# Kernel tuning notes

Hardware: AMD Instinct MI355X
Metric: run time of the kernel (lower is better)

## Reference

```python
import jax, jax.numpy as jnp
import numpy as np
from jax import lax

H = 128          # lstm hidden size
IN = 128         # time_steps == LSTM input_size
NUM_LAYERS = 3   # num_variables
B = 512          # batch
S = 512          # sequence length


def _lstm_layer(x_tbi, Wih, Whh, bih, bhh):
    """x_tbi: (T, B, in). PyTorch gate order i, f, g, o. Returns (T, B, H), (hT, cT)."""
    T, Bb, _ = x_tbi.shape
    Hh = Whh.shape[1]
    # precompute input contribution to gates outside the scan
    xg = jnp.einsum('tbi,gi->tbg', x_tbi, Wih) + bih + bhh  # (T, B, 4H)

    def step(carry, xg_t):
        h, c = carry
        g = xg_t + h @ Whh.T                                # (B, 4H)
        i, f, gg, o = jnp.split(g, 4, axis=-1)
        c = jax.nn.sigmoid(f) * c + jax.nn.sigmoid(i) * jnp.tanh(gg)
        h = jax.nn.sigmoid(o) * jnp.tanh(c)
        return (h, c), h

    h0 = jnp.zeros((Bb, Hh), x_tbi.dtype)
    c0 = jnp.zeros((Bb, Hh), x_tbi.dtype)
    (hT, cT), ys = lax.scan(step, (h0, c0), xg)
    return ys, (hT, cT)


def setup_inputs() -> dict:
    key = jax.random.key(0)
    ks = jax.random.split(key, 1 + 4 * NUM_LAYERS)
    inp = {"x": jax.random.normal(ks[0], (B, S, IN), dtype=jnp.float32)}
    k = 1.0 / np.sqrt(H)
    ki = 1
    for l in range(NUM_LAYERS):
        in_dim = IN if l == 0 else H
        inp[f"Wih{l}"] = jax.random.uniform(ks[ki], (4 * H, in_dim), jnp.float32, -k, k); ki += 1
        inp[f"Whh{l}"] = jax.random.uniform(ks[ki], (4 * H, H), jnp.float32, -k, k); ki += 1
        inp[f"bih{l}"] = jax.random.uniform(ks[ki], (4 * H,), jnp.float32, -k, k); ki += 1
        inp[f"bhh{l}"] = jax.random.uniform(ks[ki], (4 * H,), jnp.float32, -k, k); ki += 1
    return inp


def reference(x, Wih0, Whh0, bih0, bhh0, Wih1, Whh1, bih1, bhh1, Wih2, Whh2, bih2, bhh2):
    # x: (B, S, IN) -> (S, B, IN), stacked LSTM, output (S, B, H)
    h = jnp.transpose(x, (1, 0, 2))
    params = [(Wih0, Whh0, bih0, bhh0), (Wih1, Whh1, bih1, bhh1), (Wih2, Whh2, bih2, bhh2)]
    for (Wih, Whh, bih, bhh) in params:
        h, _ = _lstm_layer(h, Wih, Whh, bih, bhh)
    # y = output.transpose(1, 2): (S, B, H) -> (S, H, B); dropout is identity in eval
    return jnp.transpose(h, (0, 2, 1))
```

## Files before the change

kernel.cpp:

```cpp
#include <hip/hip_runtime.h>
#include <stdint.h>

#define BATCH 512
#define SEQ   512
#define HID   128
#define BT    16
#define ROWB  528
#define NTILE 32
#define CH    8
#define RING  64
#define FPAD  32
#define SKEW  8

typedef _Float16 half8 __attribute__((ext_vector_type(8)));
typedef float f32x4 __attribute__((ext_vector_type(4)));
typedef unsigned long long u64;

union UHP { uint32_t u; _Float16 h[2]; };
__device__ __forceinline__ uint32_t pack2f(float a, float b){
  UHP r; r.h[0] = (_Float16)a; r.h[1] = (_Float16)b; return r.u;
}
__device__ __forceinline__ float unpk(uint32_t u, int i){
  UHP r; r.u = u; return (float)r.h[i];
}

__device__ __forceinline__ float rcp_(float x){
#if __has_builtin(__builtin_amdgcn_rcpf)
  return __builtin_amdgcn_rcpf(x);
#else
  return 1.f / x;
#endif
}
__device__ __forceinline__ float exp2_(float x){
#if __has_builtin(__builtin_amdgcn_exp2f)
  return __builtin_amdgcn_exp2f(x);
#else
  return exp2f(x);
#endif
}
__device__ __forceinline__ float sigm(float x){ return rcp_(1.f + exp2_(x * -1.44269504f)); }
__device__ __forceinline__ float tanh_(float x){ return 1.f - 2.f * rcp_(exp2_(x * 2.88539008f) + 1.f); }

__device__ __forceinline__ int aload(const int* p){
  return __hip_atomic_load(p, __ATOMIC_RELAXED, __HIP_MEMORY_SCOPE_AGENT);
}

template<int MODE>
__device__ __forceinline__ void run_layer(
    const float* __restrict__ Wih, const float* __restrict__ Whh,
    const float* __restrict__ bih, const float* __restrict__ bhh,
    const float* __restrict__ x, uint32_t* __restrict__ rin,
    uint32_t* __restrict__ rout, float* __restrict__ y,
    int* src_ready, int* src_done, int* dst_ready, int* dst_done,
    int b0, char* act0, char* act1)
{
  const int tid  = threadIdx.x;
  const int lane = tid & 63;
  const int w    = tid >> 6;
  const int u0   = w * 16;
  const int rm   = lane & 15;
  const int kq   = lane >> 4;

  half8 wf[4][8];
  #pragma unroll
  for (int g = 0; g < 4; ++g){
    const int grow = g * HID + u0 + rm;
    #pragma unroll
    for (int s = 0; s < 8; ++s){
      const int k = s * 32 + kq * 8;
      const float* src = (s < 4) ? (Wih + (size_t)grow * HID + k)
                                 : (Whh + (size_t)grow * HID + (k - HID));
      const float4 aa = *(const float4*)src;
      const float4 bb = *(const float4*)(src + 4);
      half8 hh;
      hh[0]=(_Float16)aa.x; hh[1]=(_Float16)aa.y; hh[2]=(_Float16)aa.z; hh[3]=(_Float16)aa.w;
      hh[4]=(_Float16)bb.x; hh[5]=(_Float16)bb.y; hh[6]=(_Float16)bb.z; hh[7]=(_Float16)bb.w;
      wf[g][s] = hh;
    }
  }
  f32x4 bias4[4];
  #pragma unroll
  for (int g = 0; g < 4; ++g)
    #pragma unroll
    for (int r = 0; r < 4; ++r){
      const int row = g * HID + u0 + kq * 4 + r;
      bias4[g][r] = bih[row] + bhh[row];
    }

  const int sb = tid >> 5;
  const int sk = tid & 31;

  auto xaddr = [&](int t){
    return (const float4*)(x + ((size_t)(b0 + sb) * SEQ + t) * HID + sk * 4);
  };
  auto raddr = [&](int t){
    return (u64*)(rin + ((size_t)(t & (RING-1)) * BATCH + b0 + sb) * 64 + sk * 2);
  };

  float4 pfa, pfb;
  u64    pga = 0, pgb = 0;

  int fseen = 0, fpend = 0, dseen = 0;

  if constexpr (MODE != 0){
    fseen = aload(src_ready);
    while (fseen < SKEW){ __builtin_amdgcn_s_sleep(8); fseen = aload(src_ready); }
  }
  if constexpr (MODE == 0){
    const float4 v = *xaddr(0);
    uint2 p; p.x = pack2f(v.x, v.y); p.y = pack2f(v.z, v.w);
    *(uint2*)(act0 + sb * ROWB + sk * 8) = p;
    pfa = *xaddr(1);
  } else {
    const u64 v = __hip_atomic_load(raddr(0), __ATOMIC_RELAXED, __HIP_MEMORY_SCOPE_AGENT);
    *(u64*)(act0 + sb * ROWB + sk * 8) = v;
    pga = __hip_atomic_load(raddr(1), __ATOMIC_RELAXED, __HIP_MEMORY_SCOPE_AGENT);
    fpend = aload(src_ready);
  }
  if (tid < 256)
    *(uint4*)(act0 + (tid >> 4) * ROWB + 256 + (tid & 15) * 16) = make_uint4(0u,0u,0u,0u);
  __syncthreads();

  f32x4 c4 = {0.f, 0.f, 0.f, 0.f};
  const int boff = rm * ROWB + kq * 16;
  int cur = 0;

  uint2 hp = {0u, 0u};

  for (int t = 0; t < SEQ; ++t){
    char* bc = cur ? act1 : act0;
    char* bn = cur ? act0 : act1;
    const int tn   = t + 1;
    const int tpre = t + 2;

    if (t > 0){
      if constexpr (MODE != 2){
        const u64 hp64 = ((u64)hp.y << 32) | (u64)hp.x;
        u64* p = (u64*)(rout + ((size_t)((t-1) & (RING-1)) * BATCH + b0 + rm) * 64 + (u0 >> 1) + kq * 2);
        __hip_atomic_store(p, hp64, __ATOMIC_RELAXED, __HIP_MEMORY_SCOPE_AGENT);
      } else {
        const size_t yb = ((size_t)(t-1) * HID + u0 + kq * 4) * BATCH + b0 + rm;
        y[yb]             = unpk(hp.x, 0);
        y[yb + BATCH]     = unpk(hp.x, 1);
        y[yb + 2 * BATCH] = unpk(hp.y, 0);
        y[yb + 3 * BATCH] = unpk(hp.y, 1);
      }
    }
    if (tid == 0){
      if constexpr (MODE != 2){
        if (t >= 2)
          __hip_atomic_store(dst_ready, t - 1, __ATOMIC_RELAXED, __HIP_MEMORY_SCOPE_AGENT);
      }
      if constexpr (MODE != 0){
        if ((t & (CH-1)) == 0 && t > 0)
          __hip_atomic_store(src_done, t >> 3, __ATOMIC_RELAXED, __HIP_MEMORY_SCOPE_AGENT);
      }
    }
    if constexpr (MODE != 2){
      if ((t & (CH-1)) == 0 && t >= RING){
        const int need = (t >> 3) - 7;
        if (dseen < need){
          dseen = aload(dst_done);
          while (dseen < need){ __builtin_amdgcn_s_sleep(8); dseen = aload(dst_done); }
        }
      }
    }
    if constexpr (MODE != 0){
      const int fnew = fpend;
      if (fnew > fseen) fseen = fnew;
      fpend = aload(src_ready);
      if (tpre < SEQ && fseen < tpre + 1){
        fseen = aload(src_ready);
        while (fseen < tpre + 1){ __builtin_amdgcn_s_sleep(2); fseen = aload(src_ready); }
      }
    }
    if (tpre < SEQ){
      if constexpr (MODE == 0) pfb = *xaddr(tpre);
      else pgb = __hip_atomic_load(raddr(tpre), __ATOMIC_RELAXED, __HIP_MEMORY_SCOPE_AGENT);
    }

    f32x4 a0 = bias4[0], a1 = bias4[1], a2 = bias4[2], a3 = bias4[3];
    #pragma unroll
    for (int s = 0; s < 8; ++s){
      const half8 bf = *(const half8*)(bc + boff + s * 64);
      a0 = __builtin_amdgcn_mfma_f32_16x16x32_f16(wf[0][s], bf, a0, 0, 0, 0);
      a1 = __builtin_amdgcn_mfma_f32_16x16x32_f16(wf[1][s], bf, a1, 0, 0, 0);
      a2 = __builtin_amdgcn_mfma_f32_16x16x32_f16(wf[2][s], bf, a2, 0, 0, 0);
      a3 = __builtin_amdgcn_mfma_f32_16x16x32_f16(wf[3][s], bf, a3, 0, 0, 0);
    }

    float hvr[4];
    #pragma unroll
    for (int r = 0; r < 4; ++r){
      const float ii = sigm(a0[r]), ff = sigm(a1[r]);
      const float gg = tanh_(a2[r]), oo = sigm(a3[r]);
      c4[r] = ff * c4[r] + ii * gg;
      hvr[r] = oo * tanh_(c4[r]);
    }
    hp.x = pack2f(hvr[0], hvr[1]);
    hp.y = pack2f(hvr[2], hvr[3]);

    *(uint2*)(bn + rm * ROWB + 256 + u0 * 2 + kq * 8) = hp;
    if (tn < SEQ){
      if constexpr (MODE == 0){
        uint2 p; p.x = pack2f(pfa.x, pfa.y); p.y = pack2f(pfa.z, pfa.w);
        *(uint2*)(bn + sb * ROWB + sk * 8) = p;
      } else {
        *(u64*)(bn + sb * ROWB + sk * 8) = pga;
      }
    }
    __syncthreads();
    pfa = pfb; pga = pgb;
    cur ^= 1;
  }

  if constexpr (MODE != 2){
    const u64 hp64 = ((u64)hp.y << 32) | (u64)hp.x;
    u64* p = (u64*)(rout + ((size_t)((SEQ-1) & (RING-1)) * BATCH + b0 + rm) * 64 + (u0 >> 1) + kq * 2);
    __hip_atomic_store(p, hp64, __ATOMIC_RELAXED, __HIP_MEMORY_SCOPE_AGENT);
  } else {
    const size_t yb = ((size_t)(SEQ-1) * HID + u0 + kq * 4) * BATCH + b0 + rm;
    y[yb]             = unpk(hp.x, 0);
    y[yb + BATCH]     = unpk(hp.x, 1);
    y[yb + 2 * BATCH] = unpk(hp.y, 0);
    y[yb + 3 * BATCH] = unpk(hp.y, 1);
  }
  __syncthreads();
  if (tid == 0){
    if constexpr (MODE != 2)
      __hip_atomic_store(dst_ready, SEQ, __ATOMIC_RELAXED, __HIP_MEMORY_SCOPE_AGENT);
    if constexpr (MODE != 0)
      __hip_atomic_store(src_done, SEQ / CH, __ATOMIC_RELAXED, __HIP_MEMORY_SCOPE_AGENT);
  }
}

__global__ __launch_bounds__(512, 2) void lstm_pipe(
    const float* W0i, const float* W0h, const float* b0i, const float* b0h,
    const float* W1i, const float* W1h, const float* b1i, const float* b1h,
    const float* W2i, const float* W2h, const float* b2i, const float* b2h,
    const float* x, float* y, uint32_t* ring, int* flags)
{
  const int layer = blockIdx.x >> 5;
  const int tile  = blockIdx.x & 31;
  const int b0    = tile * BT;

  __shared__ char act[2][BT * ROWB];

  uint32_t* r0 = ring;
  uint32_t* r1 = ring + (size_t)RING * BATCH * 64;

  int* p0 = flags + (0 * NTILE + tile) * FPAD;
  int* p1 = flags + (1 * NTILE + tile) * FPAD;
  int* c0 = flags + (2 * NTILE + tile) * FPAD;
  int* c1 = flags + (3 * NTILE + tile) * FPAD;

  if (layer == 0){
    run_layer<0>(W0i, W0h, b0i, b0h, x, nullptr, r0, nullptr,
                 nullptr, nullptr, p0, c0, b0, act[0], act[1]);
  } else if (layer == 1){
    run_layer<1>(W1i, W1h, b1i, b1h, nullptr, r0, r1, nullptr,
                 p0, c0, p1, c1, b0, act[0], act[1]);
  } else {
    run_layer<2>(W2i, W2h, b2i, b2h, nullptr, r1, nullptr, y,
                 p1, c1, nullptr, nullptr, b0, act[0], act[1]);
  }
}

extern "C" void kernel_launch(void* const* d_in, const int* in_sizes, int n_in,
                              void* d_out, int out_size, void* d_ws, size_t ws_size,
                              hipStream_t stream) {
  const float* x    = (const float*)d_in[0];
  const float* Wih0 = (const float*)d_in[1];
  const float* Whh0 = (const float*)d_in[2];
  const float* bih0 = (const float*)d_in[3];
  const float* bhh0 = (const float*)d_in[4];
  const float* Wih1 = (const float*)d_in[5];
  const float* Whh1 = (const float*)d_in[6];
  const float* bih1 = (const float*)d_in[7];
  const float* bhh1 = (const float*)d_in[8];
  const float* Wih2 = (const float*)d_in[9];
  const float* Whh2 = (const float*)d_in[10];
  const float* bih2 = (const float*)d_in[11];
  const float* bhh2 = (const float*)d_in[12];

  float* out = (float*)d_out;
  uint32_t* ring = (uint32_t*)d_ws;
  const size_t ring_bytes = (size_t)2 * RING * BATCH * 64 * 4;
  int* flags = (int*)((char*)d_ws + ring_bytes);

  hipMemsetAsync(flags, 0, 4 * NTILE * FPAD * sizeof(int), stream);

  dim3 grid(3 * NTILE), block(512);
  lstm_pipe<<<grid, block, 0, stream>>>(
      Wih0, Whh0, bih0, bhh0, Wih1, Whh1, bih1, bhh1, Wih2, Whh2, bih2, bhh2,
      x, out, ring, flags);
}
```

Measured before the change: 657.9 us.

## Precompute next step's input-gate MFMAs off the recurrent critical path

Splits the combined [x;h] MFMA into separate input and recurrent halves. The input contribution for step t+1 is computed at the end of step t, so only the four recurrent K-chunks remain on the serial dependency chain. To support this, the x staging buffer becomes a 3-slot ring held apart from the double-buffered h buffer, and prefetch and flag waits move one step further ahead. The cost is more shared memory and more live registers, and the upstream layer must now run one step further ahead before this layer can proceed.

New measurement: 659.2 us. About the same (+0.2%).

```diff
diff --git a/kernel.cpp b/kernel.cpp
--- a/kernel.cpp
+++ b/kernel.cpp
@@ -5,7 +5,8 @@
 #define SEQ   512
 #define HID   128
 #define BT    16
-#define ROWB  528
+#define XROW  272
+#define XSZ   (BT*XROW)
 #define NTILE 32
 #define CH    8
 #define RING  64
@@ -52,7 +53,7 @@
     const float* __restrict__ x, uint32_t* __restrict__ rin,
     uint32_t* __restrict__ rout, float* __restrict__ y,
     int* src_ready, int* src_done, int* dst_ready, int* dst_done,
-    int b0, char* act0, char* act1)
+    int b0, char* xb, char* hb)
 {
   const int tid  = threadIdx.x;
   const int lane = tid & 63;
@@ -61,21 +62,25 @@
   const int rm   = lane & 15;
   const int kq   = lane >> 4;
 
-  half8 wf[4][8];
+  half8 wih[4][4], whh[4][4];
   #pragma unroll
   for (int g = 0; g < 4; ++g){
     const int grow = g * HID + u0 + rm;
     #pragma unroll
-    for (int s = 0; s < 8; ++s){
+    for (int s = 0; s < 4; ++s){
       const int k = s * 32 + kq * 8;
-      const float* src = (s < 4) ? (Wih + (size_t)grow * HID + k)
-                                 : (Whh + (size_t)grow * HID + (k - HID));
-      const float4 aa = *(const float4*)src;
-      const float4 bb = *(const float4*)(src + 4);
+      const float* si = Wih + (size_t)grow * HID + k;
+      const float* sh = Whh + (size_t)grow * HID + k;
+      float4 aa = *(const float4*)si, bb = *(const float4*)(si + 4);
+      half8 hi;
+      hi[0]=(_Float16)aa.x; hi[1]=(_Float16)aa.y; hi[2]=(_Float16)aa.z; hi[3]=(_Float16)aa.w;
+      hi[4]=(_Float16)bb.x; hi[5]=(_Float16)bb.y; hi[6]=(_Float16)bb.z; hi[7]=(_Float16)bb.w;
+      wih[g][s] = hi;
+      aa = *(const float4*)sh; bb = *(const float4*)(sh + 4);
       half8 hh;
       hh[0]=(_Float16)aa.x; hh[1]=(_Float16)aa.y; hh[2]=(_Float16)aa.z; hh[3]=(_Float16)aa.w;
       hh[4]=(_Float16)bb.x; hh[5]=(_Float16)bb.y; hh[6]=(_Float16)bb.z; hh[7]=(_Float16)bb.w;
-      wf[g][s] = hh;
+      whh[g][s] = hh;
     }
   }
   f32x4 bias4[4];
@@ -107,31 +112,46 @@
     while (fseen < SKEW){ __builtin_amdgcn_s_sleep(8); fseen = aload(src_ready); }
   }
   if constexpr (MODE == 0){
-    const float4 v = *xaddr(0);
+    float4 v = *xaddr(0);
     uint2 p; p.x = pack2f(v.x, v.y); p.y = pack2f(v.z, v.w);
-    *(uint2*)(act0 + sb * ROWB + sk * 8) = p;
-    pfa = *xaddr(1);
+    *(uint2*)(xb + sb * XROW + sk * 8) = p;
+    v = *xaddr(1);
+    p.x = pack2f(v.x, v.y); p.y = pack2f(v.z, v.w);
+    *(uint2*)(xb + XSZ + sb * XROW + sk * 8) = p;
+    pfa = *xaddr(2);
   } else {
-    const u64 v = __hip_atomic_load(raddr(0), __ATOMIC_RELAXED, __HIP_MEMORY_SCOPE_AGENT);
-    *(u64*)(act0 + sb * ROWB + sk * 8) = v;
-    pga = __hip_atomic_load(raddr(1), __ATOMIC_RELAXED, __HIP_MEMORY_SCOPE_AGENT);
+    u64 v = __hip_atomic_load(raddr(0), __ATOMIC_RELAXED, __HIP_MEMORY_SCOPE_AGENT);
+    *(u64*)(xb + sb * XROW + sk * 8) = v;
+    v = __hip_atomic_load(raddr(1), __ATOMIC_RELAXED, __HIP_MEMORY_SCOPE_AGENT);
+    *(u64*)(xb + XSZ + sb * XROW + sk * 8) = v;
+    pga = __hip_atomic_load(raddr(2), __ATOMIC_RELAXED, __HIP_MEMORY_SCOPE_AGENT);
     fpend = aload(src_ready);
   }
   if (tid < 256)
-    *(uint4*)(act0 + (tid >> 4) * ROWB + 256 + (tid & 15) * 16) = make_uint4(0u,0u,0u,0u);
+    *(uint4*)(hb + (tid >> 4) * XROW + (tid & 15) * 16) = make_uint4(0u,0u,0u,0u);
   __syncthreads();
 
+  const int foff = rm * XROW + kq * 16;
+  f32x4 a0 = bias4[0], a1 = bias4[1], a2 = bias4[2], a3 = bias4[3];
+  #pragma unroll
+  for (int s = 0; s < 4; ++s){
+    const half8 bf = *(const half8*)(xb + foff + s * 64);
+    a0 = __builtin_amdgcn_mfma_f32_16x16x32_f16(wih[0][s], bf, a0, 0, 0, 0);
+    a1 = __builtin_amdgcn_mfma_f32_16x16x32_f16(wih[1][s], bf, a1, 0, 0, 0);
+    a2 = __builtin_amdgcn_mfma_f32_16x16x32_f16(wih[2][s], bf, a2, 0, 0, 0);
+    a3 = __builtin_amdgcn_mfma_f32_16x16x32_f16(wih[3][s], bf, a3, 0, 0, 0);
+  }
+
   f32x4 c4 = {0.f, 0.f, 0.f, 0.f};
-  const int boff = rm * ROWB + kq * 16;
-  int cur = 0;
-
+  int cur = 0, xr = 1, xw = 2;
   uint2 hp = {0u, 0u};
 
   for (int t = 0; t < SEQ; ++t){
-    char* bc = cur ? act1 : act0;
-    char* bn = cur ? act0 : act1;
-    const int tn   = t + 1;
-    const int tpre = t + 2;
+    char* hbc = hb + cur * XSZ;
+    char* hbn = hb + (cur ^ 1) * XSZ;
+    char* xbr = xb + xr * XSZ;
+    char* xbw = xb + xw * XSZ;
+    const int tn = t + 1;
 
     if (t > 0){
       if constexpr (MODE != 2){
@@ -166,27 +186,25 @@
       }
     }
     if constexpr (MODE != 0){
-      const int fnew = fpend;
-      if (fnew > fseen) fseen = fnew;
+      if (fpend > fseen) fseen = fpend;
       fpend = aload(src_ready);
-      if (tpre < SEQ && fseen < tpre + 1){
+      if (t + 3 < SEQ && fseen < t + 4){
         fseen = aload(src_ready);
-        while (fseen < tpre + 1){ __builtin_amdgcn_s_sleep(2); fseen = aload(src_ready); }
-      }
-    }
-    if (tpre < SEQ){
-      if constexpr (MODE == 0) pfb = *xaddr(tpre);
-      else pgb = __hip_atomic_load(raddr(tpre), __ATOMIC_RELAXED, __HIP_MEMORY_SCOPE_AGENT);
-    }
-
-    f32x4 a0 = bias4[0], a1 = bias4[1], a2 = bias4[2], a3 = bias4[3];
+        while (fseen < t + 4){ __builtin_amdgcn_s_sleep(2); fseen = aload(src_ready); }
+      }
+    }
+    if (t + 3 < SEQ){
+      if constexpr (MODE == 0) pfb = *xaddr(t + 3);
+      else pgb = __hip_atomic_load(raddr(t + 3), __ATOMIC_RELAXED, __HIP_MEMORY_SCOPE_AGENT);
+    }
+
     #pragma unroll
-    for (int s = 0; s < 8; ++s){
-      const half8 bf = *(const half8*)(bc + boff + s * 64);
-      a0 = __builtin_amdgcn_mfma_f32_16x16x32_f16(wf[0][s], bf, a0, 0, 0, 0);
-      a1 = __builtin_amdgcn_mfma_f32_16x16x32_f16(wf[1][s], bf, a1, 0, 0, 0);
-      a2 = __builtin_amdgcn_mfma_f32_16x16x32_f16(wf[2][s], bf, a2, 0, 0, 0);
-      a3 = __builtin_amdgcn_mfma_f32_16x16x32_f16(wf[3][s], bf, a3, 0, 0, 0);
+    for (int s = 0; s < 4; ++s){
+      const half8 bf = *(const half8*)(hbc + foff + s * 64);
+      a0 = __builtin_amdgcn_mfma_f32_16x16x32_f16(whh[0][s], bf, a0, 0, 0, 0);
+      a1 = __builtin_amdgcn_mfma_f32_16x16x32_f16(whh[1][s], bf, a1, 0, 0, 0);
+      a2 = __builtin_amdgcn_mfma_f32_16x16x32_f16(whh[2][s], bf, a2, 0, 0, 0);
+      a3 = __builtin_amdgcn_mfma_f32_16x16x32_f16(whh[3][s], bf, a3, 0, 0, 0);
     }
 
     float hvr[4];
@@ -200,17 +218,33 @@
     hp.x = pack2f(hvr[0], hvr[1]);
     hp.y = pack2f(hvr[2], hvr[3]);
 
-    *(uint2*)(bn + rm * ROWB + 256 + u0 * 2 + kq * 8) = hp;
-    if (tn < SEQ){
+    *(uint2*)(hbn + rm * XROW + u0 * 2 + kq * 8) = hp;
+
+    if (t + 2 < SEQ){
       if constexpr (MODE == 0){
         uint2 p; p.x = pack2f(pfa.x, pfa.y); p.y = pack2f(pfa.z, pfa.w);
-        *(uint2*)(bn + sb * ROWB + sk * 8) = p;
+        *(uint2*)(xbw + sb * XROW + sk * 8) = p;
       } else {
-        *(u64*)(bn + sb * ROWB + sk * 8) = pga;
-      }
-    }
+        *(u64*)(xbw + sb * XROW + sk * 8) = pga;
+      }
+    }
+
+    if (tn < SEQ){
+      a0 = bias4[0]; a1 = bias4[1]; a2 = bias4[2]; a3 = bias4[3];
+      #pragma unroll
+      for (int s = 0; s < 4; ++s){
+        const half8 bf = *(const half8*)(xbr + foff + s * 64);
+        a0 = __builtin_amdgcn_mfma_f32_16x16x32_f16(wih[0][s], bf, a0, 0, 0, 0);
+        a1 = __builtin_amdgcn_mfma_f32_16x16x32_f16(wih[1][s], bf, a1, 0, 0, 0);
+        a2 = __builtin_amdgcn_mfma_f32_16x16x32_f16(wih[2][s], bf, a2, 0, 0, 0);
+        a3 = __builtin_amdgcn_mfma_f32_16x16x32_f16(wih[3][s], bf, a3, 0, 0, 0);
+      }
+    }
+
     __syncthreads();
     pfa = pfb; pga = pgb;
+    xr = (xr == 2) ? 0 : xr + 1;
+    xw = (xw == 2) ? 0 : xw + 1;
     cur ^= 1;
   }
 
@@ -244,7 +278,9 @@
   const int tile  = blockIdx.x & 31;
   const int b0    = tile * BT;
 
-  __shared__ char act[2][BT * ROWB];
+  __shared__ char smem[5 * XSZ];
+  char* xb = smem;
+  char* hb = smem + 3 * XSZ;
 
   uint32_t* r0 = ring;
   uint32_t* r1 = ring + (size_t)RING * BATCH * 64;
@@ -256,13 +292,13 @@
 
   if (layer == 0){
     run_layer<0>(W0i, W0h, b0i, b0h, x, nullptr, r0, nullptr,
-                 nullptr, nullptr, p0, c0, b0, act[0], act[1]);
+                 nullptr, nullptr, p0, c0, b0, xb, hb);
   } else if (layer == 1){
     run_layer<1>(W1i, W1h, b1i, b1h, nullptr, r0, r1, nullptr,
-                 p0, c0, p1, c1, b0, act[0], act[1]);
+                 p0, c0, p1, c1, b0, xb, hb);
   } else {
     run_layer<2>(W2i, W2h, b2i, b2h, nullptr, r1, nullptr, y,
-                 p1, c1, nullptr, nullptr, b0, act[0], act[1]);
+                 p1, c1, nullptr, nullptr, b0, xb, hb);
   }
 }
 
```
